# Kernel tuning notes

Measured on AMD Instinct MI355X. Metric: run time of the kernel, lower is better.

## Reference

```python
import jax, jax.numpy as jnp
import numpy as np

B, S, DIM, H, D = 2, 2048, 1024, 16, 64
WINDOW = 512
MAX_MEM_SEGMENTS = 1
ROPE_THETA = 10000.0


def _rope(t, pos):
    # lucidrains rotary-embedding-torch default: interleaved pairs
    d = t.shape[-1]
    inv_freq = 1.0 / (ROPE_THETA ** (jnp.arange(0, d, 2, dtype=jnp.float32) / d))
    freqs = pos[:, None].astype(jnp.float32) * inv_freq[None, :]        # [S, d/2]
    freqs = jnp.repeat(freqs, 2, axis=-1)                               # [S, d]
    cos, sin = jnp.cos(freqs), jnp.sin(freqs)
    t1, t2 = t[..., 0::2], t[..., 1::2]
    rot = jnp.stack((-t2, t1), axis=-1).reshape(t.shape)                # rotate_half
    return t * cos + rot * sin


def setup_inputs() -> dict:
    key = jax.random.key(0)
    ks = jax.random.split(key, 8)
    tokens = jax.random.normal(ks[0], (B, S, DIM), dtype=jnp.float32)
    value_residual = jax.random.normal(ks[1], (B, H, S, D), dtype=jnp.float32)
    episode_ids = jnp.sort(jax.random.randint(ks[2], (B, S), 0, 4), axis=-1)
    w = 0.02
    Wq = jax.random.normal(ks[3], (DIM, H * D), dtype=jnp.float32) * w
    Wkv = jax.random.normal(ks[4], (DIM, 2 * H * D), dtype=jnp.float32) * w
    Wo = jax.random.normal(ks[5], (H * D, DIM), dtype=jnp.float32) * w
    Wg = jax.random.normal(ks[6], (DIM, H), dtype=jnp.float32) * w
    Wmix = jax.random.normal(ks[7], (DIM, H), dtype=jnp.float32) * w
    return {"tokens": tokens, "value_residual": value_residual, "episode_ids": episode_ids,
            "Wq": Wq, "Wkv": Wkv, "Wo": Wo, "Wg": Wg, "Wmix": Wmix}


def reference(tokens, value_residual, episode_ids, Wq, Wkv, Wo, Wg, Wmix):
    b, s, _ = tokens.shape
    scale = D ** -0.5

    def split_heads(x):  # [b, n, h*d] -> [b, h, n, d]
        return x.reshape(b, s, H, D).transpose(0, 2, 1, 3)

    q = split_heads(tokens @ Wq)
    kv = tokens @ Wkv
    k, v = split_heads(kv[..., :H * D]), split_heads(kv[..., H * D:])

    q = q * scale

    # value-residual lerp: v.lerp(value_residual, mix)
    mix = jax.nn.sigmoid(jnp.einsum('bnd,dh->bhn', tokens, Wmix))[..., None]  # [b,h,n,1]
    v = v + mix * (value_residual - v)

    pos = jnp.arange(s)
    q = _rope(q, pos)
    k = _rope(k, pos)

    sim = jnp.einsum('bhid,bhjd->bhij', q, k)

    # fixed-window causal mask: masked where dist < 0 or dist > max_mem_segments*window
    dist = pos[:, None] - pos[None, :]
    win_mask = (dist < 0) | (dist > MAX_MEM_SEGMENTS * WINDOW)            # [s, s]
    ep_mask = episode_ids[:, :, None] != episode_ids[:, None, :]          # [b, s, s]
    mask = win_mask[None, None, :, :] | ep_mask[:, None, :, :]

    sim = jnp.where(mask, -jnp.finfo(sim.dtype).max, sim)
    attn = jax.nn.softmax(sim, axis=-1)
    out = jnp.einsum('bhij,bhjd->bhid', attn, v)

    # sigmoid value gating
    gate = jax.nn.sigmoid(jnp.einsum('bnd,dh->bhn', tokens, Wg))[..., None]
    out = out * gate

    out = out.transpose(0, 2, 1, 3).reshape(b, s, H * D)
    return out @ Wo
```

## Files before the change

kernel.cpp:

```cpp
#include <hip/hip_runtime.h>
#include <math.h>

#define BB 2
#define SS 2048
#define DIMM 1024
#define HH 16
#define DD 64
#define WINDOW 512

typedef __bf16 bf16x8 __attribute__((ext_vector_type(8)));
typedef float f32x4 __attribute__((ext_vector_type(4)));

__device__ __forceinline__ unsigned short f2bf(float f) {
    unsigned int u = __float_as_uint(f);
    u = (u + 0x7FFFu + ((u >> 16) & 1u)) >> 16;
    return (unsigned short)u;
}
__device__ __forceinline__ float bf2f(unsigned short u) {
    return __uint_as_float((unsigned int)u << 16);
}

__device__ __forceinline__ void async_cp16(unsigned short* lds_dst, const unsigned short* g_src) {
    __builtin_amdgcn_global_load_lds(
        (const __attribute__((address_space(1))) unsigned int*)g_src,
        (__attribute__((address_space(3))) unsigned int*)lds_dst, 16, 0, 0);
}

__global__ __launch_bounds__(256) void cvt_bf16_kernel(
    const float* __restrict__ src, unsigned short* __restrict__ dst, int n4)
{
    for (int i = blockIdx.x * 256 + threadIdx.x; i < n4; i += gridDim.x * 256) {
        float4 v = ((const float4*)src)[i];
        ushort4 o;
        o.x = f2bf(v.x); o.y = f2bf(v.y); o.z = f2bf(v.z); o.w = f2bf(v.w);
        ((ushort4*)dst)[i] = o;
    }
}

__global__ __launch_bounds__(256) void transpose_cvt_kernel(
    const float* __restrict__ src, unsigned short* __restrict__ dst, int R, int C)
{
    __shared__ float t[32][33];
    int c0 = blockIdx.x * 32, r0 = blockIdx.y * 32;
    int tx = threadIdx.x, ty = threadIdx.y;
    #pragma unroll
    for (int u = 0; u < 4; ++u)
        t[ty + 8 * u][tx] = src[(size_t)(r0 + ty + 8 * u) * C + c0 + tx];
    __syncthreads();
    #pragma unroll
    for (int u = 0; u < 4; ++u)
        dst[(size_t)(c0 + ty + 8 * u) * R + r0 + tx] = f2bf(t[tx][ty + 8 * u]);
}

__global__ __launch_bounds__(256) void build_wgmt_kernel(
    const float* __restrict__ Wg, const float* __restrict__ Wmix,
    unsigned short* __restrict__ dst)
{
    int idx = blockIdx.x * 256 + threadIdx.x;
    int n = idx >> 10, k = idx & 1023;
    const float* src = (n < 16) ? Wg : Wmix;
    dst[idx] = f2bf(src[k * HH + (n & 15)]);
}

__global__ __launch_bounds__(256) void mixgate_mfma(
    const unsigned short* __restrict__ A,
    const unsigned short* __restrict__ Bt,
    float* __restrict__ gate, float* __restrict__ mix)
{
    int mbase = blockIdx.x * 32;
    int tid = threadIdx.x;
    int wave = tid >> 6, lane = tid & 63;
    int fr = lane & 15, hi = lane >> 4;
    int kw = wave * 256;

    __shared__ float red[4][32][32];

    f32x4 acc[2][2];
    #pragma unroll
    for (int m_ = 0; m_ < 2; ++m_)
        #pragma unroll
        for (int n_ = 0; n_ < 2; ++n_)
            acc[m_][n_] = (f32x4){0.f, 0.f, 0.f, 0.f};

    const unsigned short* a0 = A + (size_t)(mbase + fr) * 1024 + kw + hi * 8;
    const unsigned short* a1 = A + (size_t)(mbase + 16 + fr) * 1024 + kw + hi * 8;
    const unsigned short* b0 = Bt + (size_t)fr * 1024 + kw + hi * 8;
    const unsigned short* b1 = Bt + (size_t)(16 + fr) * 1024 + kw + hi * 8;

    #pragma unroll 2
    for (int k = 0; k < 256; k += 32) {
        bf16x8 af0 = *(const bf16x8*)(a0 + k);
        bf16x8 af1 = *(const bf16x8*)(a1 + k);
        bf16x8 bf0 = *(const bf16x8*)(b0 + k);
        bf16x8 bf1 = *(const bf16x8*)(b1 + k);
        acc[0][0] = __builtin_amdgcn_mfma_f32_16x16x32_bf16(af0, bf0, acc[0][0], 0, 0, 0);
        acc[0][1] = __builtin_amdgcn_mfma_f32_16x16x32_bf16(af0, bf1, acc[0][1], 0, 0, 0);
        acc[1][0] = __builtin_amdgcn_mfma_f32_16x16x32_bf16(af1, bf0, acc[1][0], 0, 0, 0);
        acc[1][1] = __builtin_amdgcn_mfma_f32_16x16x32_bf16(af1, bf1, acc[1][1], 0, 0, 0);
    }

    #pragma unroll
    for (int m_ = 0; m_ < 2; ++m_)
        #pragma unroll
        for (int n_ = 0; n_ < 2; ++n_)
            #pragma unroll
            for (int j = 0; j < 4; ++j)
                red[wave][m_ * 16 + hi * 4 + j][n_ * 16 + fr] = acc[m_][n_][j];
    __syncthreads();

    #pragma unroll
    for (int e = 0; e < 4; ++e) {
        int idx = (tid << 2) | e;
        int r = idx >> 5, c = idx & 31;
        float s4 = red[0][r][c] + red[1][r][c] + red[2][r][c] + red[3][r][c];
        float sg = 1.f / (1.f + __expf(-s4));
        int mg = mbase + r;
        int b = mg >> 11, s = mg & 2047;
        int h = c & 15;
        float* dst = (c < 16) ? gate : mix;
        dst[((size_t)b * HH + h) * SS + s] = sg;
    }
}

__global__ __launch_bounds__(256) void epstart_kernel(
    const int* __restrict__ ep, int* __restrict__ epstart)
{
    int idx = blockIdx.x * 256 + threadIdx.x;
    int b = idx >> 11, i = idx & 2047;
    const int* e = ep + b * SS;
    int v = e[i];
    int lo = 0, hi = i;
    while (lo < hi) {
        int mid = (lo + hi) >> 1;
        if (e[mid] == v) hi = mid; else lo = mid + 1;
    }
    epstart[idx] = lo;
}

template<int EPI, int BN>
__global__ __launch_bounds__(256) void gemm_mfma(
    const unsigned short* __restrict__ A, const unsigned short* __restrict__ Bt,
    void* __restrict__ o0v, void* __restrict__ o1v, void* __restrict__ o2v)
{
    const int K = 1024;
    constexpr int NFR = BN / 32;
    int nbase = blockIdx.x * BN;
    int mbase = blockIdx.y * 128;
    int tid = threadIdx.x;
    int lane = tid & 63;
    int wave = tid >> 6;
    int wr = wave >> 1, wc = wave & 1;
    int fr = lane & 15, hi = lane >> 4;

    __shared__ unsigned short As[2][128 * 32];
    __shared__ unsigned short Bs[2][BN * 32];

    int srow = tid >> 2;
    int sp   = tid & 3;
    int scol = (sp ^ ((srow >> 1) & 3)) * 8;
    const unsigned short* agp0 = A  + (size_t)(mbase + srow) * K + scol;
    const unsigned short* agp1 = A  + (size_t)(mbase + srow + 64) * K + scol;
    const unsigned short* bgp0 = Bt + (size_t)(nbase + srow) * K + scol;
    const unsigned short* bgp1 = (BN == 128)
        ? Bt + (size_t)(nbase + srow + 64) * K + scol : bgp0;

    f32x4 acc[4][NFR];
    #pragma unroll
    for (int m_ = 0; m_ < 4; ++m_)
        #pragma unroll
        for (int n_ = 0; n_ < NFR; ++n_)
            acc[m_][n_] = (f32x4){0.f, 0.f, 0.f, 0.f};

    int aidx[4], bidx[NFR];
    #pragma unroll
    for (int m_ = 0; m_ < 4; ++m_) {
        int row = wr * 64 + m_ * 16 + fr;
        aidx[m_] = row * 32 + (hi ^ ((row >> 1) & 3)) * 8;
    }
    #pragma unroll
    for (int n_ = 0; n_ < NFR; ++n_) {
        int row = wc * (BN / 2) + n_ * 16 + fr;
        bidx[n_] = row * 32 + (hi ^ ((row >> 1) & 3)) * 8;
    }

    auto stage = [&](int buf, int k0) {
        async_cp16(&As[buf][tid * 8], agp0 + k0);
        async_cp16(&As[buf][2048 + tid * 8], agp1 + k0);
        async_cp16(&Bs[buf][tid * 8], bgp0 + k0);
        if constexpr (BN == 128)
            async_cp16(&Bs[buf][2048 + tid * 8], bgp1 + k0);
    };

    stage(0, 0);
    for (int k0 = 0; k0 < K; k0 += 32) {
        int cur = (k0 >> 5) & 1;
        __syncthreads();
        if (k0 + 32 < K) stage(cur ^ 1, k0 + 32);

        bf16x8 af[4], bfr[NFR];
        #pragma unroll
        for (int m_ = 0; m_ < 4; ++m_) af[m_] = *(const bf16x8*)&As[cur][aidx[m_]];
        #pragma unroll
        for (int n_ = 0; n_ < NFR; ++n_) bfr[n_] = *(const bf16x8*)&Bs[cur][bidx[n_]];
        #pragma unroll
        for (int m_ = 0; m_ < 4; ++m_)
            #pragma unroll
            for (int n_ = 0; n_ < NFR; ++n_)
                acc[m_][n_] = __builtin_amdgcn_mfma_f32_16x16x32_bf16(
                    af[m_], bfr[n_], acc[m_][n_], 0, 0, 0);
    }

    #pragma unroll
    for (int m_ = 0; m_ < 4; ++m_) {
        #pragma unroll
        for (int n_ = 0; n_ < NFR; ++n_) {
            int c = nbase + wc * (BN / 2) + n_ * 16 + fr;
            #pragma unroll
            for (int j = 0; j < 4; ++j) {
                int mg = mbase + wr * 64 + m_ * 16 + hi * 4 + j;
                float v = acc[m_][n_][j];
                if (EPI == 0) {
                    ((float*)o0v)[(size_t)mg * 1024 + c] = v;
                } else {
                    int b = mg >> 11, s = mg & 2047;
                    int cc = c & 1023, h = cc >> 6, d = cc & 63;
                    unsigned short* dst = (c < 1024) ? (unsigned short*)o0v
                                        : (c < 2048) ? (unsigned short*)o1v
                                                     : (unsigned short*)o2v;
                    dst[(((size_t)b * HH + h) * SS + s) * DD + d] = f2bf(v);
                }
            }
        }
    }
}

__global__ __launch_bounds__(256) void rope_lerp_kernel(
    unsigned short* __restrict__ q, unsigned short* __restrict__ k,
    const unsigned short* __restrict__ v0, const float* __restrict__ vres,
    const float* __restrict__ mix, unsigned short* __restrict__ vt)
{
    int st = blockIdx.x;
    int bh = blockIdx.y;
    int tid = threadIdx.x;
    int sl = tid >> 2;
    int dg = (tid & 3) * 16;
    int s = st * 64 + sl;
    size_t rowoff = ((size_t)bh * SS + s) * DD + dg;

    __shared__ unsigned short vtile[64][66];

    union { uint4 v[2]; unsigned short u[16]; } qa, ka, va;
    qa.v[0] = *(const uint4*)(q + rowoff);
    qa.v[1] = *(const uint4*)(q + rowoff + 8);
    ka.v[0] = *(const uint4*)(k + rowoff);
    ka.v[1] = *(const uint4*)(k + rowoff + 8);
    va.v[0] = *(const uint4*)(v0 + rowoff);
    va.v[1] = *(const uint4*)(v0 + rowoff + 8);
    float4 w[4];
    #pragma unroll
    for (int u = 0; u < 4; ++u) w[u] = *(const float4*)(vres + rowoff + 4 * u);
    float mx = mix[(size_t)bh * SS + s];

    #pragma unroll
    for (int u = 0; u < 8; ++u) {
        int d0 = dg + 2 * u;
        float inv_freq = powf(10000.f, -(float)d0 * (1.f / 64.f));
        float fr = (float)s * inv_freq;
        float red = fr - 6.2831853f * floorf(fr * 0.15915494f);
        float cs, sn;
        __sincosf(red, &sn, &cs);
        float x = bf2f(qa.u[2 * u]), y = bf2f(qa.u[2 * u + 1]);
        qa.u[2 * u]     = f2bf((x * cs - y * sn) * 0.125f);
        qa.u[2 * u + 1] = f2bf((y * cs + x * sn) * 0.125f);
        x = bf2f(ka.u[2 * u]); y = bf2f(ka.u[2 * u + 1]);
        ka.u[2 * u]     = f2bf(x * cs - y * sn);
        ka.u[2 * u + 1] = f2bf(y * cs + x * sn);
    }
    *(uint4*)(q + rowoff)     = qa.v[0];
    *(uint4*)(q + rowoff + 8) = qa.v[1];
    *(uint4*)(k + rowoff)     = ka.v[0];
    *(uint4*)(k + rowoff + 8) = ka.v[1];

    #pragma unroll
    for (int e = 0; e < 16; ++e) {
        float vv = bf2f(va.u[e]);
        float wr = ((const float*)w)[e];
        vtile[sl][dg + e] = f2bf(vv + mx * (wr - vv));
    }
    __syncthreads();

    int d = tid >> 2;
    int sseg = (tid & 3) * 16;
    union { uint4 v[2]; unsigned short u[16]; } ot;
    #pragma unroll
    for (int e = 0; e < 16; ++e) ot.u[e] = vtile[sseg + e][d];
    unsigned short* dst = vt + ((size_t)bh * DD + d) * SS + st * 64 + sseg;
    *(uint4*)dst = ot.v[0];
    *(uint4*)(dst + 8) = ot.v[1];
}

__global__ __launch_bounds__(256) void attn_mfma(
    const unsigned short* __restrict__ qbh, const unsigned short* __restrict__ kbh,
    const unsigned short* __restrict__ vt, const int* __restrict__ epstart,
    const float* __restrict__ gate, unsigned short* __restrict__ ao)
{
    int orig = blockIdx.x;
    int swz  = (orig & 7) * 128 + (orig >> 3);
    int bh = swz >> 5, qt = swz & 31;
    int b = bh >> 4, h = bh & 15;
    int q0 = qt * 64;
    int tid = threadIdx.x;
    int wave = tid >> 6, lane = tid & 63;
    int lq = lane & 15, lg = lane >> 4;
    int i = q0 + wave * 16 + lq;

    __shared__ unsigned short Ks[4096];
    __shared__ unsigned short Vs[4096];
    alignas(16) __shared__ unsigned short P_lds[4][16][72];

    int srow0 = tid >> 3, sch = tid & 7;
    int srow1 = srow0 + 32;
    int sc0 = ((sch ^ (srow0 & 7)) << 3);
    int sc1 = ((sch ^ (srow1 & 7)) << 3);
    const unsigned short* kS0 = kbh + ((size_t)bh * SS + srow0) * DD + sc0;
    const unsigned short* kS1 = kbh + ((size_t)bh * SS + srow1) * DD + sc1;
    const unsigned short* vS0 = vt + ((size_t)bh * DD + srow0) * SS + sc0;
    const unsigned short* vS1 = vt + ((size_t)bh * DD + srow1) * SS + sc1;
    unsigned short* kd0 = &Ks[tid * 8];
    unsigned short* kd1 = &Ks[2048 + tid * 8];
    unsigned short* vd0 = &Vs[tid * 8];
    unsigned short* vd1 = &Vs[2048 + tid * 8];

    int fidx[4];
    #pragma unroll
    for (int n = 0; n < 4; ++n) {
        int r = 16 * n + lq;
        fidx[n] = r * 64 + ((lg ^ (r & 7)) << 3);
    }

    const unsigned short* qrow = qbh + ((size_t)bh * SS + i) * DD + lg * 8;
    bf16x8 bq0 = *(const bf16x8*)qrow;
    bf16x8 bq1 = *(const bf16x8*)(qrow + 32);

    int jmin = i - WINDOW;
    int es = epstart[b * SS + i];
    if (es > jmin) jmin = es;
    float gi = gate[(size_t)bh * SS + i];

    float m = -1e30f, l = 0.f;
    f32x4 o[4];
    #pragma unroll
    for (int n = 0; n < 4; ++n) o[n] = (f32x4){0.f, 0.f, 0.f, 0.f};

    int t0 = (qt < 8) ? (8 - qt) : 0;
    for (int t = t0; t < 9; ++t) {
        int jbase = 64 * (qt - 8 + t);

        __syncthreads();
        async_cp16(kd0, kS0 + (size_t)jbase * DD);
        async_cp16(kd1, kS1 + (size_t)jbase * DD);
        async_cp16(vd0, vS0 + jbase);
        async_cp16(vd1, vS1 + jbase);
        __syncthreads();

        f32x4 acc[4];
        #pragma unroll
        for (int n = 0; n < 4; ++n) acc[n] = (f32x4){0.f, 0.f, 0.f, 0.f};
        #pragma unroll
        for (int n = 0; n < 4; ++n) {
            bf16x8 kf0 = *(const bf16x8*)&Ks[fidx[n]];
            bf16x8 kf1 = *(const bf16x8*)&Ks[fidx[n] ^ 32];
            acc[n] = __builtin_amdgcn_mfma_f32_16x16x32_bf16(kf0, bq0, acc[n], 0, 0, 0);
            acc[n] = __builtin_amdgcn_mfma_f32_16x16x32_bf16(kf1, bq1, acc[n], 0, 0, 0);
        }

        int jb = jbase + lg * 4;
        #pragma unroll
        for (int n = 0; n < 4; ++n)
            #pragma unroll
            for (int r = 0; r < 4; ++r) {
                int j = jb + 16 * n + r;
                if (j < jmin || j > i) acc[n][r] = -3e38f;
            }

        float tm = -3e38f;
        #pragma unroll
        for (int n = 0; n < 4; ++n)
            tm = fmaxf(tm, fmaxf(fmaxf(acc[n][0], acc[n][1]), fmaxf(acc[n][2], acc[n][3])));
        tm = fmaxf(tm, __shfl_xor(tm, 16, 64));
        tm = fmaxf(tm, __shfl_xor(tm, 32, 64));
        float mnew = fmaxf(m, tm);
        float scale = __expf(m - mnew);
        float ts = 0.f;
        #pragma unroll
        for (int n = 0; n < 4; ++n)
            #pragma unroll
            for (int r = 0; r < 4; ++r) {
                float p = __expf(acc[n][r] - mnew);
                acc[n][r] = p;
                ts += p;
            }
        ts += __shfl_xor(ts, 16, 64);
        ts += __shfl_xor(ts, 32, 64);
        l = l * scale + ts;
        m = mnew;
        #pragma unroll
        for (int n = 0; n < 4; ++n) o[n] = o[n] * scale;

        #pragma unroll
        for (int n = 0; n < 4; ++n) {
            ushort4 u;
            u.x = f2bf(acc[n][0]); u.y = f2bf(acc[n][1]);
            u.z = f2bf(acc[n][2]); u.w = f2bf(acc[n][3]);
            *(ushort4*)&P_lds[wave][lq][16 * n + lg * 4] = u;
        }
        bf16x8 bp0 = *(const bf16x8*)&P_lds[wave][lq][lg * 8];
        bf16x8 bp1 = *(const bf16x8*)&P_lds[wave][lq][32 + lg * 8];

        #pragma unroll
        for (int n = 0; n < 4; ++n) {
            bf16x8 vf0 = *(const bf16x8*)&Vs[fidx[n]];
            bf16x8 vf1 = *(const bf16x8*)&Vs[fidx[n] ^ 32];
            o[n] = __builtin_amdgcn_mfma_f32_16x16x32_bf16(vf0, bp0, o[n], 0, 0, 0);
            o[n] = __builtin_amdgcn_mfma_f32_16x16x32_bf16(vf1, bp1, o[n], 0, 0, 0);
        }
    }

    float g = gi / l;
    #pragma unroll
    for (int n = 0; n < 4; ++n) {
        ushort4 u;
        u.x = f2bf(o[n][0] * g); u.y = f2bf(o[n][1] * g);
        u.z = f2bf(o[n][2] * g); u.w = f2bf(o[n][3] * g);
        *(ushort4*)(ao + (((size_t)b * SS + i) * HH + h) * DD + 16 * n + lg * 4) = u;
    }
}

extern "C" void kernel_launch(void* const* d_in, const int* in_sizes, int n_in,
                              void* d_out, int out_size, void* d_ws, size_t ws_size,
                              hipStream_t stream)
{
    const float* tokens = (const float*)d_in[0];
    const float* vres   = (const float*)d_in[1];
    const int*   ep     = (const int*)d_in[2];
    const float* Wq     = (const float*)d_in[3];
    const float* Wkv    = (const float*)d_in[4];
    const float* Wo     = (const float*)d_in[5];
    const float* Wg     = (const float*)d_in[6];
    const float* Wmix   = (const float*)d_in[7];
    float* out = (float*)d_out;

    char* wsb = (char*)d_ws;
    unsigned short* qbh  = (unsigned short*)(wsb + 0);
    unsigned short* kbh  = (unsigned short*)(wsb + 8388608);
    unsigned short* vb0  = (unsigned short*)(wsb + 16777216);
    unsigned short* vtb  = (unsigned short*)(wsb + 25165824);
    unsigned short* aob  = (unsigned short*)(wsb + 33554432);
    unsigned short* tokA = (unsigned short*)(wsb + 41943040);
    unsigned short* BtW  = (unsigned short*)(wsb + 50331648);
    unsigned short* WotW = BtW;
    float* gatep = (float*)(wsb + 56623104);
    float* mixp  = (float*)(wsb + 56885248);
    int*   epst  = (int*)(wsb + 57147392);
    unsigned short* wgmt = (unsigned short*)(wsb + 57163776);

    cvt_bf16_kernel<<<2048, 256, 0, stream>>>(tokens, tokA, (BB * SS * DIMM) / 4);
    transpose_cvt_kernel<<<dim3(32, 32), dim3(32, 8), 0, stream>>>(Wq,  BtW,               1024, 1024);
    transpose_cvt_kernel<<<dim3(64, 32), dim3(32, 8), 0, stream>>>(Wkv, BtW + 1024 * 1024, 1024, 2048);
    build_wgmt_kernel<<<128, 256, 0, stream>>>(Wg, Wmix, wgmt);
    epstart_kernel<<<16, 256, 0, stream>>>(ep, epst);

    mixgate_mfma<<<128, 256, 0, stream>>>(tokA, wgmt, gatep, mixp);
    gemm_mfma<1, 128><<<dim3(24, 32), 256, 0, stream>>>(tokA, BtW, qbh, kbh, vb0);
    rope_lerp_kernel<<<dim3(SS / 64, BB * HH), 256, 0, stream>>>(qbh, kbh, vb0, vres, mixp, vtb);
    attn_mfma<<<1024, 256, 0, stream>>>(qbh, kbh, vtb, epst, gatep, aob);

    transpose_cvt_kernel<<<dim3(32, 32), dim3(32, 8), 0, stream>>>(Wo, WotW, 1024, 1024);
    gemm_mfma<0, 64><<<dim3(16, 32), 256, 0, stream>>>(aob, WotW, out, nullptr, nullptr);
}
```

Before: 128.0 us.

## Deepen async LDS pipelines in GEMM and attention with vmcnt-based waits

The GEMM moves from double to quad buffering with three stages in flight. It waits on explicit vmcnt counts plus a single raw barrier instead of two __syncthreads per step. The attention kernel gets a triple-buffered K/V pipeline that prefetches two tiles ahead, replacing the load-then-sync pattern that exposed global latency every tile. This costs more LDS, which may lower occupancy, and makes correctness depend on the hand-counted vmcnt values.

```diff
diff --git a/kernel.cpp b/kernel.cpp
--- a/kernel.cpp
+++ b/kernel.cpp
@@ -143,6 +143,7 @@
     void* __restrict__ o0v, void* __restrict__ o1v, void* __restrict__ o2v)
 {
     const int K = 1024;
+    const int NT = 32;
     constexpr int NFR = BN / 32;
     int nbase = blockIdx.x * BN;
     int mbase = blockIdx.y * 128;
@@ -152,8 +153,8 @@
     int wr = wave >> 1, wc = wave & 1;
     int fr = lane & 15, hi = lane >> 4;
 
-    __shared__ unsigned short As[2][128 * 32];
-    __shared__ unsigned short Bs[2][BN * 32];
+    __shared__ unsigned short As[4][128 * 32];
+    __shared__ unsigned short Bs[4][BN * 32];
 
     int srow = tid >> 2;
     int sp   = tid & 3;
@@ -190,24 +191,34 @@
         if constexpr (BN == 128)
             async_cp16(&Bs[buf][2048 + tid * 8], bgp1 + k0);
     };
-
-    stage(0, 0);
-    for (int k0 = 0; k0 < K; k0 += 32) {
-        int cur = (k0 >> 5) & 1;
-        __syncthreads();
-        if (k0 + 32 < K) stage(cur ^ 1, k0 + 32);
-
+    auto compute = [&](int buf) {
         bf16x8 af[4], bfr[NFR];
         #pragma unroll
-        for (int m_ = 0; m_ < 4; ++m_) af[m_] = *(const bf16x8*)&As[cur][aidx[m_]];
-        #pragma unroll
-        for (int n_ = 0; n_ < NFR; ++n_) bfr[n_] = *(const bf16x8*)&Bs[cur][bidx[n_]];
+        for (int m_ = 0; m_ < 4; ++m_) af[m_] = *(const bf16x8*)&As[buf][aidx[m_]];
+        #pragma unroll
+        for (int n_ = 0; n_ < NFR; ++n_) bfr[n_] = *(const bf16x8*)&Bs[buf][bidx[n_]];
         #pragma unroll
         for (int m_ = 0; m_ < 4; ++m_)
             #pragma unroll
             for (int n_ = 0; n_ < NFR; ++n_)
                 acc[m_][n_] = __builtin_amdgcn_mfma_f32_16x16x32_bf16(
                     af[m_], bfr[n_], acc[m_][n_], 0, 0, 0);
+    };
+
+    stage(0, 0); stage(1, 32); stage(2, 64);
+    for (int t = 0; t < NT; ++t) {
+        if (t + 2 < NT) {
+            if constexpr (BN == 128) asm volatile("s_waitcnt vmcnt(8)" ::: "memory");
+            else                     asm volatile("s_waitcnt vmcnt(6)" ::: "memory");
+        } else if (t + 1 < NT) {
+            if constexpr (BN == 128) asm volatile("s_waitcnt vmcnt(4)" ::: "memory");
+            else                     asm volatile("s_waitcnt vmcnt(3)" ::: "memory");
+        } else {
+            asm volatile("s_waitcnt vmcnt(0)" ::: "memory");
+        }
+        __builtin_amdgcn_s_barrier();
+        if (t + 3 < NT) stage((t + 3) & 3, (t + 3) * 32);
+        compute(t & 3);
     }
 
     #pragma unroll
@@ -314,8 +325,8 @@
     int lq = lane & 15, lg = lane >> 4;
     int i = q0 + wave * 16 + lq;
 
-    __shared__ unsigned short Ks[4096];
-    __shared__ unsigned short Vs[4096];
+    __shared__ unsigned short Ks[3][4096];
+    __shared__ unsigned short Vs[3][4096];
     alignas(16) __shared__ unsigned short P_lds[4][16][72];
 
     int srow0 = tid >> 3, sch = tid & 7;
@@ -326,10 +337,13 @@
     const unsigned short* kS1 = kbh + ((size_t)bh * SS + srow1) * DD + sc1;
     const unsigned short* vS0 = vt + ((size_t)bh * DD + srow0) * SS + sc0;
     const unsigned short* vS1 = vt + ((size_t)bh * DD + srow1) * SS + sc1;
-    unsigned short* kd0 = &Ks[tid * 8];
-    unsigned short* kd1 = &Ks[2048 + tid * 8];
-    unsigned short* vd0 = &Vs[tid * 8];
-    unsigned short* vd1 = &Vs[2048 + tid * 8];
+
+    auto stageKV = [&](int buf, int jbase) {
+        async_cp16(&Ks[buf][tid * 8],        kS0 + (size_t)jbase * DD);
+        async_cp16(&Ks[buf][2048 + tid * 8], kS1 + (size_t)jbase * DD);
+        async_cp16(&Vs[buf][tid * 8],        vS0 + jbase);
+        async_cp16(&Vs[buf][2048 + tid * 8], vS1 + jbase);
+    };
 
     int fidx[4];
     #pragma unroll
@@ -353,23 +367,27 @@
     for (int n = 0; n < 4; ++n) o[n] = (f32x4){0.f, 0.f, 0.f, 0.f};
 
     int t0 = (qt < 8) ? (8 - qt) : 0;
-    for (int t = t0; t < 9; ++t) {
-        int jbase = 64 * (qt - 8 + t);
-
-        __syncthreads();
-        async_cp16(kd0, kS0 + (size_t)jbase * DD);
-        async_cp16(kd1, kS1 + (size_t)jbase * DD);
-        async_cp16(vd0, vS0 + jbase);
-        async_cp16(vd1, vS1 + jbase);
-        __syncthreads();
+    int nt = 9 - t0;
+    int jb0 = 64 * (qt - 8 + t0);
+
+    stageKV(0, jb0);
+    if (nt > 1) stageKV(1, jb0 + 64);
+
+    for (int u = 0; u < nt; ++u) {
+        if (u + 1 < nt) asm volatile("s_waitcnt vmcnt(4)" ::: "memory");
+        else            asm volatile("s_waitcnt vmcnt(0)" ::: "memory");
+        __builtin_amdgcn_s_barrier();
+        if (u + 2 < nt) stageKV((u + 2) % 3, jb0 + 64 * (u + 2));
+        int buf = u % 3;
+        int jbase = jb0 + 64 * u;
 
         f32x4 acc[4];
         #pragma unroll
         for (int n = 0; n < 4; ++n) acc[n] = (f32x4){0.f, 0.f, 0.f, 0.f};
         #pragma unroll
         for (int n = 0; n < 4; ++n) {
-            bf16x8 kf0 = *(const bf16x8*)&Ks[fidx[n]];
-            bf16x8 kf1 = *(const bf16x8*)&Ks[fidx[n] ^ 32];
+            bf16x8 kf0 = *(const bf16x8*)&Ks[buf][fidx[n]];
+            bf16x8 kf1 = *(const bf16x8*)&Ks[buf][fidx[n] ^ 32];
             acc[n] = __builtin_amdgcn_mfma_f32_16x16x32_bf16(kf0, bq0, acc[n], 0, 0, 0);
             acc[n] = __builtin_amdgcn_mfma_f32_16x16x32_bf16(kf1, bq1, acc[n], 0, 0, 0);
         }
@@ -409,18 +427,18 @@
 
         #pragma unroll
         for (int n = 0; n < 4; ++n) {
-            ushort4 u;
-            u.x = f2bf(acc[n][0]); u.y = f2bf(acc[n][1]);
-            u.z = f2bf(acc[n][2]); u.w = f2bf(acc[n][3]);
-            *(ushort4*)&P_lds[wave][lq][16 * n + lg * 4] = u;
+            ushort4 u4;
+            u4.x = f2bf(acc[n][0]); u4.y = f2bf(acc[n][1]);
+            u4.z = f2bf(acc[n][2]); u4.w = f2bf(acc[n][3]);
+            *(ushort4*)&P_lds[wave][lq][16 * n + lg * 4] = u4;
         }
         bf16x8 bp0 = *(const bf16x8*)&P_lds[wave][lq][lg * 8];
         bf16x8 bp1 = *(const bf16x8*)&P_lds[wave][lq][32 + lg * 8];
 
         #pragma unroll
         for (int n = 0; n < 4; ++n) {
-            bf16x8 vf0 = *(const bf16x8*)&Vs[fidx[n]];
-            bf16x8 vf1 = *(const bf16x8*)&Vs[fidx[n] ^ 32];
+            bf16x8 vf0 = *(const bf16x8*)&Vs[buf][fidx[n]];
+            bf16x8 vf1 = *(const bf16x8*)&Vs[buf][fidx[n] ^ 32];
             o[n] = __builtin_amdgcn_mfma_f32_16x16x32_bf16(vf0, bp0, o[n], 0, 0, 0);
             o[n] = __builtin_amdgcn_mfma_f32_16x16x32_bf16(vf1, bp1, o[n], 0, 0, 0);
         }
@@ -429,10 +447,10 @@
     float g = gi / l;
     #pragma unroll
     for (int n = 0; n < 4; ++n) {
-        ushort4 u;
-        u.x = f2bf(o[n][0] * g); u.y = f2bf(o[n][1] * g);
-        u.z = f2bf(o[n][2] * g); u.w = f2bf(o[n][3] * g);
-        *(ushort4*)(ao + (((size_t)b * SS + i) * HH + h) * DD + 16 * n + lg * 4) = u;
+        ushort4 u4;
+        u4.x = f2bf(o[n][0] * g); u4.y = f2bf(o[n][1] * g);
+        u4.z = f2bf(o[n][2] * g); u4.w = f2bf(o[n][3] * g);
+        *(ushort4*)(ao + (((size_t)b * SS + i) * HH + h) * DD + 16 * n + lg * 4) = u4;
     }
 }
 
```

New measurement: 141.9 us. 10.9% more time.
